# Performance work log

Measured on AMD Instinct MI355X. Metric: run time of the kernel, lower is better.

Reference implementation:

```python
import jax, jax.numpy as jnp
import numpy as np

N_USER = 805   # herbs
N_ITEM = 390   # symptoms
N = 1195       # total nodes
D = 64         # embedding_dim (forced by final matmul)
E = 1_000_000
E_SUB = 500_000
B = 2048
BN_EPS = 1e-5


def _gcn(x, W, b, edge):
    # GCNConv_SH: message = Linear(x_j), aggr='mean', then tanh.
    # Linear commutes with mean (bias included when in-degree>0; isolated nodes -> 0),
    # so transform nodes once, then gather->segment-mean.
    h = x @ W.T + b                      # [N, D]
    src, dst = edge[0], edge[1]
    agg = jax.ops.segment_sum(h[src], dst, num_segments=N)          # [N, D]
    cnt = jax.ops.segment_sum(jnp.ones(edge.shape[1], x.dtype), dst, num_segments=N)
    mean = agg / jnp.maximum(cnt, 1.0)[:, None]   # isolated nodes stay 0 (PyG mean aggr)
    return jnp.tanh(mean)


def _two_layer(x, W1, b1, W2, b2, edge):
    return _gcn(_gcn(x, W1, b1, edge), W2, b2, edge)


def _norm(x, axis):
    # self.Norm(emb, count, n_dim): L2 normalize along n_dim (0 for user side, 1 for item side)
    return x / jnp.linalg.norm(x, axis=axis, keepdims=True)


def setup_inputs() -> dict:
    key = jax.random.key(0)
    ks = jax.random.split(key, 12)
    emb = jax.random.normal(ks[0], (N, D), jnp.float32)
    s = 1.0 / np.sqrt(D)
    W1 = jax.random.normal(ks[1], (D, D), jnp.float32) * s
    b1 = jnp.zeros((D,), jnp.float32)
    W2 = jax.random.normal(ks[2], (D, D), jnp.float32) * s
    b2 = jnp.zeros((D,), jnp.float32)
    mlp_W = jax.random.normal(ks[3], (64, D), jnp.float32) * s
    mlp_b = jnp.zeros((64,), jnp.float32)
    bn_gamma = jnp.ones((64,), jnp.float32)
    bn_beta = jnp.zeros((64,), jnp.float32)
    # multi-hot prescription; guarantee nonzero row sums for the mean-pool divide
    presc = (jax.random.uniform(ks[4], (B, N_ITEM)) < 0.05).astype(jnp.float32)
    presc = presc.at[:, 0].set(1.0)
    total_g = jax.random.randint(ks[5], (2, E), 0, N)
    sub_g1 = jax.random.randint(ks[6], (2, E_SUB), 0, N)
    sub_g2 = jax.random.randint(ks[7], (2, E_SUB), 0, N)
    edge_index_SH = jax.random.randint(ks[8], (2, 1000), 0, N)
    return {"edge_index_SH": edge_index_SH, "prescription": presc,
            "emb": emb, "W1": W1, "b1": b1, "W2": W2, "b2": b2,
            "mlp_W": mlp_W, "mlp_b": mlp_b, "bn_gamma": bn_gamma, "bn_beta": bn_beta,
            "total_g": total_g, "sub_g1": sub_g1, "sub_g2": sub_g2}


def reference(edge_index_SH, prescription, emb, W1, b1, W2, b2, mlp_W, mlp_b,
              bn_gamma, bn_beta, total_g, sub_g1, sub_g2):
    # edge_index_SH is accepted (forward signature) but unused, as in the source.
    x_SH1 = emb                                   # SH_embedding(arange(1195))
    x_SH6 = _two_layer(emb, W1, b1, W2, b2, total_g)   # two shared GCNConv_SH layers
    SH_g3 = _two_layer(emb, W1, b1, W2, b2, sub_g1)
    SH_g33 = _two_layer(emb, W1, b1, W2, b2, sub_g2)

    # ssl_layer_loss returns normalized previous (raw-embedding) views
    s_u = _norm(x_SH1[:N_USER], 0)   # [805, D]
    s_i = _norm(x_SH1[N_USER:], 1)   # [390, D]
    # sgl_loss returns normalized sub-graph-1 views
    n_u = _norm(SH_g3[:N_USER], 0)
    n_i = _norm(SH_g3[N_USER:], 1)
    # Same2Loss (reconstructed): fuse all contrastive views into final node reps
    c_u = 0.25 * (s_i + n_i + _norm(x_SH6[N_USER:], 1) + _norm(SH_g33[N_USER:], 1))  # [390, D]
    c_i = 0.25 * (s_u + n_u + _norm(x_SH6[:N_USER], 0) + _norm(SH_g33[:N_USER], 0))  # [805, D]

    e_synd = prescription @ c_u                           # [B, D]
    e_synd = e_synd / prescription.sum(axis=1, keepdims=True)
    h = e_synd @ mlp_W.T + mlp_b                          # [B, 64]
    mu = h.mean(axis=0)
    var = h.var(axis=0)                                   # biased, as torch BN training
    h = (h - mu) / jnp.sqrt(var + BN_EPS) * bn_gamma + bn_beta
    h = jax.nn.relu(h)
    pre = h @ c_i.T                                       # [B, 805]
    return pre
```

## Files before the change

### kernel.cpp

```cpp
#include <hip/hip_runtime.h>
#include <hip/hip_bf16.h>


#define NN    1195
#define NUSER 805
#define NITEM 390
#define DD    64
#define BB    2048
#define NPAD  1216
#define E_TOT 1000000
#define E_SUB 500000
#define MT    19
#define KT    8
#define CHUNK 3
#define LSTR  72
#define OUT2STRIDE (NN*DD)
#define CPG    299
#define P8W    152
#define ROWS   96
#define RB     13
#define FNT    13
#define KPAD   448
#define ENT    7

typedef unsigned int uint;
typedef unsigned short u16;
typedef unsigned char u8;
typedef __attribute__((ext_vector_type(8))) short short8;
typedef __attribute__((ext_vector_type(4))) float f32x4;

__device__ __forceinline__ float wsum(float v) {
#pragma unroll
    for (int m = 32; m > 0; m >>= 1) v += __shfl_xor(v, m, 64);
    return v;
}
__device__ __forceinline__ u16 f2b(float f) {
    uint u = __float_as_uint(f);
    return (u16)((u + 0x7FFFu + ((u >> 16) & 1u)) >> 16);
}
__device__ __forceinline__ float b2f16(u16 b) { return __uint_as_float(((uint)b) << 16); }

#define CVT_EMB   0
#define CVT_W1    76480
#define CVT_B1    80576
#define CVT_W2    80640
#define CVT_B2    84736
#define CVT_MLPW  84800
#define CVT_MLPB  88896
#define CVT_GAMMA 88960
#define CVT_BETA  89024
#define CVT_TOTAL 89088

constexpr size_t alignUp64(size_t x) { return (x + 63) & ~size_t(63); }
constexpr size_t OFF_BNS  = 0;
constexpr size_t OFF_CNSS = 128;
constexpr size_t MEMSET_FLOATS = 384;
constexpr size_t OFF_FLAG = 384;
constexpr size_t OFF_CVT  = 448;
constexpr size_t OFF_ABF  = alignUp64(OFF_CVT + CVT_TOTAL);
constexpr size_t OFF_RC   = alignUp64(OFF_ABF + (3ull * NN * NPAD) / 2);
constexpr size_t OFF_POOL = alignUp64(OFF_RC + 3ull * NPAD);
constexpr size_t OFF_PART = OFF_POOL;
constexpr size_t OFF_H1   = alignUp64(OFF_PART + (size_t)KT * 3 * NPAD * 64);
constexpr size_t OFF_H2   = alignUp64(OFF_H1 + 64ull * NPAD);
constexpr size_t OFF_OUT2 = alignUp64(OFF_H2 + 3ull * 64 * NPAD);
constexpr size_t OFF_CU   = alignUp64(OFF_OUT2 + 3ull * NN * DD);
constexpr size_t OFF_CI   = alignUp64(OFF_CU + 448ull * DD);
constexpr size_t OFF_H    = alignUp64(OFF_CI + (size_t)NUSER * DD);
constexpr size_t POOL_END = alignUp64(OFF_H + (size_t)BB * DD);


__global__ __launch_bounds__(256) void k_cvt_all(const void* presc,
        const void* p1, const void* p2, const void* p3, const void* p4,
        const void* p5, const void* p6, const void* p7, const void* p8, const void* p9,
        float* __restrict__ dst, float* __restrict__ cnss, int* __restrict__ flag) {
    int isbf = (((const u16*)presc)[0] == 0x3F80u) ? 1 : 0;
    int t = threadIdx.x;
    int i = blockIdx.x * 256 + t;
    if (i == 0) *flag = isbf;
    const void* s2; int o2;
    if      (i < CVT_W1)    { s2 = p1; o2 = i; }
    else if (i < CVT_B1)    { s2 = p2; o2 = i - CVT_W1; }
    else if (i < CVT_W2)    { s2 = p3; o2 = i - CVT_B1; }
    else if (i < CVT_B2)    { s2 = p4; o2 = i - CVT_W2; }
    else if (i < CVT_MLPW)  { s2 = p5; o2 = i - CVT_B2; }
    else if (i < CVT_MLPB)  { s2 = p6; o2 = i - CVT_MLPW; }
    else if (i < CVT_GAMMA) { s2 = p7; o2 = i - CVT_MLPB; }
    else if (i < CVT_BETA)  { s2 = p8; o2 = i - CVT_GAMMA; }
    else                    { s2 = p9; o2 = i - CVT_BETA; }
    float v = isbf ? __bfloat162float(((const __hip_bfloat16*)s2)[o2])
                   : ((const float*)s2)[o2];
    dst[i] = v;
    float x2 = (i < NUSER * 64) ? v * v : 0.0f;
    __shared__ float sd[256];
    sd[t] = x2;
    __syncthreads();
    if (t < 64 && blockIdx.x * 256 < NUSER * 64) {
        float s = sd[t] + sd[t + 64] + sd[t + 128] + sd[t + 192];
        if (s != 0.0f) atomicAdd(&cnss[t], s);
    }
}

__global__ __launch_bounds__(512) void k_histp(const int* __restrict__ tg,
        const int* __restrict__ s1, const int* __restrict__ s2,
        uint* __restrict__ P8, int S) {
    __shared__ __align__(16) uint lds[ROWS * P8W];
    int b = blockIdx.x;
    int p = b % S;
    int rg = b / S;
    int r = rg % RB;
    int g = rg / RB;
    int r0 = r * ROWS;
    int t = threadIdx.x;

    {
        uint4* l4 = (uint4*)lds;
        for (int i = t; i < (ROWS * P8W) >> 2; i += 512) l4[i] = (uint4){0u, 0u, 0u, 0u};
    }
    __syncthreads();

    const int* eg = (g == 0) ? tg : (g == 1 ? s1 : s2);
    int Eg = (g == 0) ? E_TOT : E_SUB;
    int e0 = (int)(((long)p * Eg / S) & ~3L);
    int e1 = (p == S - 1) ? Eg : (int)(((long)(p + 1) * Eg / S) & ~3L);
    const int* srcp = eg;
    const int* dstp = eg + Eg;
    for (int i = e0 + t * 4; i < e1; i += 512 * 4) {
        int4 d4 = *(const int4*)(dstp + i);
        int4 s4 = *(const int4*)(srcp + i);
        int rw;
        rw = d4.x - r0; if ((unsigned)rw < ROWS) atomicAdd(&lds[rw * P8W + (s4.x >> 3)], 1u << ((s4.x & 7) * 4));
        rw = d4.y - r0; if ((unsigned)rw < ROWS) atomicAdd(&lds[rw * P8W + (s4.y >> 3)], 1u << ((s4.y & 7) * 4));
        rw = d4.z - r0; if ((unsigned)rw < ROWS) atomicAdd(&lds[rw * P8W + (s4.z >> 3)], 1u << ((s4.z & 7) * 4));
        rw = d4.w - r0; if ((unsigned)rw < ROWS) atomicAdd(&lds[rw * P8W + (s4.w >> 3)], 1u << ((s4.w & 7) * 4));
    }
    __syncthreads();

    int rmax = ROWS; if (r0 + rmax > NN) rmax = NN - r0;
    uint* out = P8 + ((size_t)p * 3 + g) * NN * P8W + (size_t)r0 * P8W;
    int n4 = (rmax * P8W) >> 2;
    const uint4* l4 = (const uint4*)lds;
    uint4* o4 = (uint4*)out;
    for (int i = t; i < n4; i += 512) o4[i] = l4[i];
}

__global__ __launch_bounds__(256) void k_abfrc(const uint* __restrict__ P8, int S,
        u16* __restrict__ Abf, float* __restrict__ rcnt) {
    int row = blockIdx.x;
    int g = row / NN, m = row % NN;
    int t = threadIdx.x, w = t >> 6;
    float partial = 0.0f;
    if (t < P8W) {
        uint cnt[8] = {0, 0, 0, 0, 0, 0, 0, 0};
        for (int p = 0; p < S; ++p) {
            uint v = P8[(((size_t)p * 3 + g) * NN + m) * P8W + t];
#pragma unroll
            for (int k = 0; k < 8; ++k) cnt[k] += (v >> (4 * k)) & 15u;
        }
        uint4 o;
        o.x = (uint)f2b((float)cnt[0]) | ((uint)f2b((float)cnt[1]) << 16);
        o.y = (uint)f2b((float)cnt[2]) | ((uint)f2b((float)cnt[3]) << 16);
        o.z = (uint)f2b((float)cnt[4]) | ((uint)f2b((float)cnt[5]) << 16);
        o.w = (uint)f2b((float)cnt[6]) | ((uint)f2b((float)cnt[7]) << 16);
        *(uint4*)(Abf + (size_t)row * NPAD + t * 8) = o;
#pragma unroll
        for (int k = 0; k < 8; ++k) partial += (float)cnt[k];
    }
    partial = wsum(partial);
    __shared__ float ws4[4];
    if ((t & 63) == 0) ws4[w] = partial;
    __syncthreads();
    if (t == 0)
        rcnt[g * NPAD + m] = 1.0f / fmaxf(ws4[0] + ws4[1] + ws4[2] + ws4[3], 1.0f);
}

__global__ __launch_bounds__(256) void k_xf2(const float* __restrict__ xsrc,
        size_t xgstride, int ngb, int rowlim,
        const float* __restrict__ W, const float* __restrict__ bias,
        u16* __restrict__ Hhi, u16* __restrict__ Hlo, size_t hgstride, int ostride) {
    int b = blockIdx.x;
    int g = b / ngb, nt = b % ngb;
    int n0 = nt * 64;
    int t = threadIdx.x, w = t >> 6, l = t & 63;
    __shared__ u16 Ah[64 * LSTR], Al[64 * LSTR], Bh[64 * LSTR], Bl[64 * LSTR];
    __shared__ float bs[64];
    if (t < 64) bs[t] = bias ? bias[t] : 0.0f;
    int r = t >> 2, c0 = (t & 3) * 16;
    {
        const float* Wr = W + r * 64 + c0;
        int node = n0 + r;
        const float* Xr = xsrc + xgstride * g + (size_t)node * 64 + c0;
        bool xv = node < rowlim;
#pragma unroll
        for (int j = 0; j < 4; ++j) {
            float4 wv = *(const float4*)(Wr + j * 4);
            float4 xw = xv ? *(const float4*)(Xr + j * 4) : (float4){0.f, 0.f, 0.f, 0.f};
            float a4[4] = {wv.x, wv.y, wv.z, wv.w};
            float b4[4] = {xw.x, xw.y, xw.z, xw.w};
            u16 ah[4], al[4], bh[4], bl[4];
#pragma unroll
            for (int jj = 0; jj < 4; ++jj) {
                ah[jj] = f2b(a4[jj]); al[jj] = f2b(a4[jj] - b2f16(ah[jj]));
                bh[jj] = f2b(b4[jj]); bl[jj] = f2b(b4[jj] - b2f16(bh[jj]));
            }
            uint2 pa, pb, pc, pd;
            pa.x = (uint)ah[0] | ((uint)ah[1] << 16); pa.y = (uint)ah[2] | ((uint)ah[3] << 16);
            pb.x = (uint)al[0] | ((uint)al[1] << 16); pb.y = (uint)al[2] | ((uint)al[3] << 16);
            pc.x = (uint)bh[0] | ((uint)bh[1] << 16); pc.y = (uint)bh[2] | ((uint)bh[3] << 16);
            pd.x = (uint)bl[0] | ((uint)bl[1] << 16); pd.y = (uint)bl[2] | ((uint)bl[3] << 16);
            int off = r * LSTR + c0 + j * 4;
            *(uint2*)(Ah + off) = pa;
            *(uint2*)(Al + off) = pb;
            *(uint2*)(Bh + off) = pc;
            *(uint2*)(Bl + off) = pd;
        }
    }
    __syncthreads();
    f32x4 acc[4];
#pragma unroll
    for (int p = 0; p < 4; ++p) acc[p] = (f32x4){0.f, 0.f, 0.f, 0.f};
    int mrow = w * 16 + (l & 15);
    int q8 = (l >> 4) * 8;
#pragma unroll
    for (int ks = 0; ks < 2; ++ks) {
        short8 ah = *(const short8*)(Ah + mrow * LSTR + ks * 32 + q8);
        short8 al = *(const short8*)(Al + mrow * LSTR + ks * 32 + q8);
#pragma unroll
        for (int p = 0; p < 4; ++p) {
            int nrow = p * 16 + (l & 15);
            short8 bh = *(const short8*)(Bh + nrow * LSTR + ks * 32 + q8);
            short8 bl = *(const short8*)(Bl + nrow * LSTR + ks * 32 + q8);
            acc[p] = __builtin_amdgcn_mfma_f32_16x16x32_bf16(ah, bh, acc[p], 0, 0, 0);
            acc[p] = __builtin_amdgcn_mfma_f32_16x16x32_bf16(ah, bl, acc[p], 0, 0, 0);
            acc[p] = __builtin_amdgcn_mfma_f32_16x16x32_bf16(al, bh, acc[p], 0, 0, 0);
        }
    }
    int q = l >> 4;
#pragma unroll
    for (int p = 0; p < 4; ++p) {
        int node = n0 + p * 16 + (l & 15);
#pragma unroll
        for (int rr2 = 0; rr2 < 4; ++rr2) {
            int d = w * 16 + q * 4 + rr2;
            float v = acc[p][rr2] + bs[d];
            u16 h = f2b(v);
            size_t o = hgstride * g + (size_t)d * ostride + node;
            Hhi[o] = h;
            Hlo[o] = f2b(v - b2f16(h));
        }
    }
}

__global__ __launch_bounds__(256) void k_aggp(const u16* __restrict__ Abf,
        const u16* __restrict__ Hhi, const u16* __restrict__ Hlo, size_t hstride,
        float* __restrict__ part) {
    int b = blockIdx.x;
    int kt = b & 7;
    int mt = (b >> 3) % MT;
    int g  = (b >> 3) / MT;
    int t = threadIdx.x, w = t >> 6, l = t & 63;
    __shared__ u16 As[64 * LSTR], Bh[64 * LSTR], Bl[64 * LSTR];
    f32x4 acc[4];
#pragma unroll
    for (int p = 0; p < 4; ++p) acc[p] = (f32x4){0.f, 0.f, 0.f, 0.f};
    int m0 = mt * 64;
    const u16* Ag = Abf + (size_t)g * NN * NPAD;
    const u16* Hg = Hhi + hstride * g;
    const u16* Lg = Hlo + hstride * g;
    int st0 = kt * CHUNK;
    int st1 = st0 + CHUNK; if (st1 > MT) st1 = MT;
    int rr = t >> 4, c4 = (t & 15) * 4;
    for (int st = st0; st < st1; ++st) {
        int s0 = st * 64;
        __syncthreads();
#pragma unroll
        for (int pass = 0; pass < 4; ++pass) {
            int r = pass * 16 + rr;
            uint2 av = {0u, 0u};
            if (m0 + r < NN) av = *(const uint2*)(Ag + (size_t)(m0 + r) * NPAD + s0 + c4);
            *(uint2*)(As + r * LSTR + c4) = av;
            *(uint2*)(Bh + r * LSTR + c4) = *(const uint2*)(Hg + (size_t)r * NPAD + s0 + c4);
            *(uint2*)(Bl + r * LSTR + c4) = *(const uint2*)(Lg + (size_t)r * NPAD + s0 + c4);
        }
        __syncthreads();
        int mrow = w * 16 + (l & 15);
        int q8 = (l >> 4) * 8;
#pragma unroll
        for (int ks = 0; ks < 2; ++ks) {
            short8 a = *(const short8*)(As + mrow * LSTR + ks * 32 + q8);
#pragma unroll
            for (int p = 0; p < 4; ++p) {
                int nrow = p * 16 + (l & 15);
                short8 bh = *(const short8*)(Bh + nrow * LSTR + ks * 32 + q8);
                short8 bl = *(const short8*)(Bl + nrow * LSTR + ks * 32 + q8);
                acc[p] = __builtin_amdgcn_mfma_f32_16x16x32_bf16(a, bh, acc[p], 0, 0, 0);
                acc[p] = __builtin_amdgcn_mfma_f32_16x16x32_bf16(a, bl, acc[p], 0, 0, 0);
            }
        }
    }
    int q = l >> 4;
#pragma unroll
    for (int p = 0; p < 4; ++p) {
        int n = p * 16 + (l & 15);
#pragma unroll
        for (int r = 0; r < 4; ++r) {
            int m = m0 + w * 16 + q * 4 + r;
            if (m < NN)
                part[(((size_t)kt * 3 + g) * NPAD + m) * 64 + n] = acc[p][r];
        }
    }
}

__global__ __launch_bounds__(256) void k_comb1(const float* __restrict__ part,
        const float* __restrict__ rcnt, float* __restrict__ h1) {
    int g = blockIdx.x / CPG, bi = blockIdx.x % CPG;
    int idx = bi * 256 + threadIdx.x;
    if (idx >= NN * 64) return;
    int m = idx >> 6;
    float s = 0.0f;
#pragma unroll
    for (int k = 0; k < KT; ++k)
        s += part[(((size_t)k * 3 + g) * NPAD + m) * 64 + (idx & 63)];
    h1[(size_t)g * NN * 64 + idx] = tanhf(s * rcnt[g * NPAD + m]);
}

__global__ __launch_bounds__(256) void k_comb(const float* __restrict__ part,
        const float* __restrict__ rcnt, float* __restrict__ out, float* __restrict__ cnss) {
    int g = blockIdx.x / CPG, bi = blockIdx.x % CPG;
    int t = threadIdx.x;
    int idx = bi * 256 + t;
    int m = idx >> 6, n = idx & 63;
    bool valid = idx < NN * 64;
    float v = 0.0f;
    if (valid) {
        float s = 0.0f;
#pragma unroll
        for (int k = 0; k < KT; ++k)
            s += part[(((size_t)k * 3 + g) * NPAD + m) * 64 + n];
        v = tanhf(s * rcnt[g * NPAD + m]);
        out[(size_t)g * NN * 64 + idx] = v;
    }
    float x2 = (valid && m < NUSER) ? v * v : 0.0f;
    __shared__ float sd[256];
    sd[t] = x2;
    __syncthreads();
    if (t < 64) {
        float s = sd[t] + sd[t + 64] + sd[t + 128] + sd[t + 192];
        if (s != 0.0f) atomicAdd(&cnss[(g + 1) * 64 + t], s);
    }
}

__global__ void k_cuci(const float* __restrict__ embf, const float* __restrict__ out2,
                       const float* __restrict__ cnss, float* __restrict__ cu,
                       float* __restrict__ ci) {
    int b = blockIdx.x, l = threadIdx.x;
    if (b < 448) {
        if (b >= NITEM) { cu[(size_t)b * DD + l] = 0.0f; return; }
        int node = NUSER + b;
        const float* v0 = embf + (size_t)node * DD;
        const float* v1 = out2 + (size_t)node * DD;
        const float* v2 = out2 + OUT2STRIDE + (size_t)node * DD;
        const float* v3 = out2 + 2ull * OUT2STRIDE + (size_t)node * DD;
        float total = 0.0f;
        { float x = v0[l]; float ss = wsum(x * x); total += x / sqrtf(ss); }
        { float x = v1[l]; float ss = wsum(x * x); total += x / sqrtf(ss); }
        { float x = v2[l]; float ss = wsum(x * x); total += x / sqrtf(ss); }
        { float x = v3[l]; float ss = wsum(x * x); total += x / sqrtf(ss); }
        cu[(size_t)b * DD + l] = 0.25f * total;
    } else {
        int u = b - 448;
        size_t i = (size_t)u * DD + l;
        float s = embf[i] / sqrtf(cnss[l])
                + out2[i] / sqrtf(cnss[64 + l])
                + out2[OUT2STRIDE + i] / sqrtf(cnss[128 + l])
                + out2[2ull * OUT2STRIDE + i] / sqrtf(cnss[192 + l]);
        ci[i] = 0.25f * s;
    }
}

__global__ __launch_bounds__(256) void k_esynd(const void* __restrict__ presc,
        const u16* __restrict__ cwh, const u16* __restrict__ cwl,
        const float* __restrict__ mlpB, const int* __restrict__ flag,
        float* __restrict__ hpre, float* __restrict__ bnsum) {
    int m0 = blockIdx.x * 64;
    int t = threadIdx.x, w = t >> 6, l = t & 63;
    int isbf = *flag;
    const u16* pB = (const u16*)presc;
    const float* pF = (const float*)presc;
    __shared__ u16 As[64 * LSTR], Bh[64 * LSTR], Bl[64 * LSTR];
    __shared__ u16 Ones[16 * LSTR];
    __shared__ float bs[64];
    __shared__ float r1[4][64], r2[4][64];
    for (int i = t; i < 16 * LSTR; i += 256) Ones[i] = (i < 64) ? 0x3F80u : 0u;
    if (t < 64) bs[t] = mlpB[t];

    f32x4 acc[4], acc1;
#pragma unroll
    for (int p = 0; p < 4; ++p) acc[p] = (f32x4){0.f, 0.f, 0.f, 0.f};
    acc1 = (f32x4){0.f, 0.f, 0.f, 0.f};

    int rr = t >> 4, c4 = (t & 15) * 4;
    for (int st = 0; st < ENT; ++st) {
        int s0 = st * 64;
        __syncthreads();
#pragma unroll
        for (int pass = 0; pass < 4; ++pass) {
            int r = pass * 16 + rr;
            int m = m0 + r;
            int kb = s0 + c4;
            u16 a4[4];
            if (kb + 3 < NITEM) {
                if (isbf) {
                    const uint* p32 = (const uint*)pB + (((size_t)m * NITEM + kb) >> 1);
                    uint u0 = p32[0], u1 = p32[1];
                    a4[0] = (u16)u0; a4[1] = (u16)(u0 >> 16);
                    a4[2] = (u16)u1; a4[3] = (u16)(u1 >> 16);
                } else {
                    const float2* pf2 = (const float2*)(pF + (size_t)m * NITEM + kb);
                    float2 f0 = pf2[0], f1 = pf2[1];
                    a4[0] = f2b(f0.x); a4[1] = f2b(f0.y);
                    a4[2] = f2b(f1.x); a4[3] = f2b(f1.y);
                }
            } else {
#pragma unroll
                for (int j = 0; j < 4; ++j) {
                    int k = kb + j;
                    a4[j] = (k < NITEM)
                          ? (isbf ? pB[(size_t)m * NITEM + k] : f2b(pF[(size_t)m * NITEM + k]))
                          : (u16)0;
                }
            }
            uint2 o;
            o.x = (uint)a4[0] | ((uint)a4[1] << 16);
            o.y = (uint)a4[2] | ((uint)a4[3] << 16);
            *(uint2*)(As + r * LSTR + c4) = o;
            *(uint2*)(Bh + r * LSTR + c4) = *(const uint2*)(cwh + (size_t)r * KPAD + s0 + c4);
            *(uint2*)(Bl + r * LSTR + c4) = *(const uint2*)(cwl + (size_t)r * KPAD + s0 + c4);
        }
        __syncthreads();
        int mrow = w * 16 + (l & 15);
        int q8 = (l >> 4) * 8;
#pragma unroll
        for (int ks = 0; ks < 2; ++ks) {
            short8 a = *(const short8*)(As + mrow * LSTR + ks * 32 + q8);
            short8 on = *(const short8*)(Ones + (l & 15) * LSTR + ks * 32 + q8);
            acc1 = __builtin_amdgcn_mfma_f32_16x16x32_bf16(a, on, acc1, 0, 0, 0);
#pragma unroll
            for (int p = 0; p < 4; ++p) {
                int nrow = p * 16 + (l & 15);
                short8 bh = *(const short8*)(Bh + nrow * LSTR + ks * 32 + q8);
                short8 bl = *(const short8*)(Bl + nrow * LSTR + ks * 32 + q8);
                acc[p] = __builtin_amdgcn_mfma_f32_16x16x32_bf16(a, bh, acc[p], 0, 0, 0);
                acc[p] = __builtin_amdgcn_mfma_f32_16x16x32_bf16(a, bl, acc[p], 0, 0, 0);
            }
        }
    }
    float inv[4];
#pragma unroll
    for (int r = 0; r < 4; ++r)
        inv[r] = 1.0f / __shfl(acc1[r], l & 48, 64);
    int q = l >> 4;
#pragma unroll
    for (int p = 0; p < 4; ++p) {
        int col = p * 16 + (l & 15);
        float a = 0.0f, c = 0.0f;
#pragma unroll
        for (int r = 0; r < 4; ++r) {
            float hv = acc[p][r] * inv[r] + bs[col];
            hpre[(size_t)(m0 + w * 16 + q * 4 + r) * DD + col] = hv;
            a += hv; c = fmaf(hv, hv, c);
        }
        a += __shfl_xor(a, 16, 64); a += __shfl_xor(a, 32, 64);
        c += __shfl_xor(c, 16, 64); c += __shfl_xor(c, 32, 64);
        if (l < 16) { r1[w][col] = a; r2[w][col] = c; }
    }
    __syncthreads();
    if (t < 64) {
        atomicAdd(&bnsum[t],      r1[0][t] + r1[1][t] + r1[2][t] + r1[3][t]);
        atomicAdd(&bnsum[64 + t], r2[0][t] + r2[1][t] + r2[2][t] + r2[3][t]);
    }
}

__global__ __launch_bounds__(256) void k_final(const float* __restrict__ hpre,
        const float* __restrict__ bnsum, const float* __restrict__ gamma,
        const float* __restrict__ beta, const float* __restrict__ ci,
        void* __restrict__ out, const int* __restrict__ flag) {
    int b = blockIdx.x;
    int mt = b / FNT, nt = b % FNT;
    int m0 = mt * 64, n0 = nt * 64;
    int t = threadIdx.x, w = t >> 6, l = t & 63;
    __shared__ u16 Ah[64 * LSTR], Al[64 * LSTR], Bh[64 * LSTR], Bl[64 * LSTR];
    __shared__ float mn[64], rsg[64], bt[64];
    if (t < 64) {
        float mean = bnsum[t] * (1.0f / BB);
        float var = bnsum[64 + t] * (1.0f / BB) - mean * mean;
        mn[t] = mean;
        rsg[t] = gamma[t] / sqrtf(var + 1e-5f);
        bt[t] = beta[t];
    }
    __syncthreads();
    const float4* hp4 = (const float4*)(hpre + (size_t)m0 * 64);
    const float4* ci4 = (const float4*)ci;
#pragma unroll
    for (int k = 0; k < 4; ++k) {
        int i = t + k * 256;
        int r = i >> 4, c4 = (i & 15) * 4;
        float4 v = hp4[i];
        float vv[4] = {v.x, v.y, v.z, v.w};
        u16 hh[4], ll[4];
#pragma unroll
        for (int j = 0; j < 4; ++j) {
            int d = c4 + j;
            float x = fmaxf((vv[j] - mn[d]) * rsg[d] + bt[d], 0.0f);
            u16 hb = f2b(x);
            hh[j] = hb;
            ll[j] = f2b(x - b2f16(hb));
        }
        uint2 ph, pl;
        ph.x = (uint)hh[0] | ((uint)hh[1] << 16);
        ph.y = (uint)hh[2] | ((uint)hh[3] << 16);
        pl.x = (uint)ll[0] | ((uint)ll[1] << 16);
        pl.y = (uint)ll[2] | ((uint)ll[3] << 16);
        *(uint2*)(Ah + r * LSTR + c4) = ph;
        *(uint2*)(Al + r * LSTR + c4) = pl;
        int col = n0 + r;
        float4 cv = (col < NUSER) ? ci4[(size_t)col * 16 + (i & 15)]
                                  : (float4){0.f, 0.f, 0.f, 0.f};
        float cc[4] = {cv.x, cv.y, cv.z, cv.w};
#pragma unroll
        for (int j = 0; j < 4; ++j) {
            u16 hb = f2b(cc[j]);
            hh[j] = hb;
            ll[j] = f2b(cc[j] - b2f16(hb));
        }
        ph.x = (uint)hh[0] | ((uint)hh[1] << 16);
        ph.y = (uint)hh[2] | ((uint)hh[3] << 16);
        pl.x = (uint)ll[0] | ((uint)ll[1] << 16);
        pl.y = (uint)ll[2] | ((uint)ll[3] << 16);
        *(uint2*)(Bh + r * LSTR + c4) = ph;
        *(uint2*)(Bl + r * LSTR + c4) = pl;
    }
    __syncthreads();
    f32x4 acc[4];
#pragma unroll
    for (int p = 0; p < 4; ++p) acc[p] = (f32x4){0.f, 0.f, 0.f, 0.f};
    int mrow = w * 16 + (l & 15);
    int q8 = (l >> 4) * 8;
#pragma unroll
    for (int ks = 0; ks < 2; ++ks) {
        short8 ah = *(const short8*)(Ah + mrow * LSTR + ks * 32 + q8);
        short8 al = *(const short8*)(Al + mrow * LSTR + ks * 32 + q8);
#pragma unroll
        for (int p = 0; p < 4; ++p) {
            int nrow = p * 16 + (l & 15);
            short8 bh = *(const short8*)(Bh + nrow * LSTR + ks * 32 + q8);
            short8 bl = *(const short8*)(Bl + nrow * LSTR + ks * 32 + q8);
            acc[p] = __builtin_amdgcn_mfma_f32_16x16x32_bf16(ah, bh, acc[p], 0, 0, 0);
            acc[p] = __builtin_amdgcn_mfma_f32_16x16x32_bf16(ah, bl, acc[p], 0, 0, 0);
            acc[p] = __builtin_amdgcn_mfma_f32_16x16x32_bf16(al, bh, acc[p], 0, 0, 0);
        }
    }
    int isbf = *flag;
    int q = l >> 4;
#pragma unroll
    for (int p = 0; p < 4; ++p) {
        int col = n0 + p * 16 + (l & 15);
        if (col < NUSER) {
#pragma unroll
            for (int r = 0; r < 4; ++r) {
                int row = m0 + w * 16 + q * 4 + r;
                size_t o = (size_t)row * NUSER + col;
                if (isbf) ((__hip_bfloat16*)out)[o] = __float2bfloat16(acc[p][r]);
                else      ((float*)out)[o] = acc[p][r];
            }
        }
    }
}

extern "C" void kernel_launch(void* const* d_in, const int* in_sizes, int n_in,
                              void* d_out, int out_size, void* d_ws, size_t ws_size,
                              hipStream_t stream) {
    const void* presc = d_in[1];
    const void* emb   = d_in[2];
    const void* W1    = d_in[3];
    const void* b1    = d_in[4];
    const void* W2    = d_in[5];
    const void* b2    = d_in[6];
    const void* mlpW  = d_in[7];
    const void* mlpB  = d_in[8];
    const void* gamma = d_in[9];
    const void* beta  = d_in[10];
    const int* tg = (const int*)d_in[11];
    const int* s1 = (const int*)d_in[12];
    const int* s2 = (const int*)d_in[13];
    float* ws = (float*)d_ws;
    (void)in_sizes; (void)n_in; (void)out_size;

    float* bnsum = ws + OFF_BNS;
    float* cnss  = ws + OFF_CNSS;
    int*   flag  = (int*)(ws + OFF_FLAG);
    float* cvt   = ws + OFF_CVT;
    float* embF  = cvt + CVT_EMB;
    float* W1F   = cvt + CVT_W1;
    float* b1F   = cvt + CVT_B1;
    float* W2F   = cvt + CVT_W2;
    float* b2F   = cvt + CVT_B2;
    float* mlpWF = cvt + CVT_MLPW;
    float* mlpBF = cvt + CVT_MLPB;
    float* gamF  = cvt + CVT_GAMMA;
    float* betF  = cvt + CVT_BETA;
    u16*   Abf   = (u16*)(ws + OFF_ABF);
    float* rcnt  = ws + OFF_RC;
    uint*  P8    = (uint*)(ws + OFF_POOL);
    float* part  = ws + OFF_PART;
    u16*   H1hi  = (u16*)(ws + OFF_H1);
    u16*   H1lo  = H1hi + 64ull * NPAD;
    u16*   H2hi  = (u16*)(ws + OFF_H2);
    u16*   H2lo  = H2hi + 3ull * 64 * NPAD;
    float* out2  = ws + OFF_OUT2;
    float* cu    = ws + OFF_CU;
    float* ci    = ws + OFF_CI;
    float* hpre  = ws + OFF_H;
    u16*   cwh   = (u16*)(ws + OFF_PART);
    u16*   cwl   = cwh + 64ull * KPAD;

    size_t p8per = 3ull * NN * P8W;
    int S = 4;
    if      (ws_size >= (OFF_POOL + 16ull * p8per) * 4) S = 16;
    else if (ws_size >= (OFF_POOL +  8ull * p8per) * 4) S = 8;

    hipMemsetAsync(ws, 0, MEMSET_FLOATS * sizeof(float), stream);
    k_cvt_all<<<CVT_TOTAL / 256, 256, 0, stream>>>(
        presc, emb, W1, b1, W2, b2, mlpW, mlpB, gamma, beta, cvt, cnss, flag);

    k_histp<<<3 * RB * S, 512, 0, stream>>>(tg, s1, s2, P8, S);
    k_abfrc<<<3 * NN, 256, 0, stream>>>(P8, S, Abf, rcnt);

    k_xf2<<<MT, 256, 0, stream>>>(embF, 0, MT, NN, W1F, b1F, H1hi, H1lo, 0, NPAD);
    k_aggp<<<3 * MT * KT, 256, 0, stream>>>(Abf, H1hi, H1lo, 0, part);
    k_comb1<<<3 * CPG, 256, 0, stream>>>(part, rcnt, out2);
    k_xf2<<<3 * MT, 256, 0, stream>>>(out2, (size_t)NN * 64, MT, NN, W2F, b2F,
                                      H2hi, H2lo, 64ull * NPAD, NPAD);
    k_aggp<<<3 * MT * KT, 256, 0, stream>>>(Abf, H2hi, H2lo, 64ull * NPAD, part);
    k_comb<<<3 * CPG, 256, 0, stream>>>(part, rcnt, out2, cnss);

    k_cuci<<<448 + NUSER, 64, 0, stream>>>(embF, out2, cnss, cu, ci);
    k_xf2<<<ENT, 256, 0, stream>>>(cu, 0, ENT, 448, mlpWF, nullptr, cwh, cwl, 0, KPAD);

    k_esynd<<<BB / 64, 256, 0, stream>>>(presc, cwh, cwl, mlpBF, flag, hpre, bnsum);
    k_final<<<(BB / 64) * FNT, 256, 0, stream>>>(hpre, bnsum, gamF, betF, ci, d_out, flag);
}
```

Baseline: 215.9 us.

## Fuse front-end kernels and fold layer-1 combine into second transform

Merges the memset, conversion, histogram and embedding-norm work into one heterogeneous front kernel. It also fuses adjacency-to-bf16 conversion with the first linear transform, and folds the layer-1 partial reduction plus tanh into the layer-2 transform's input load. The intent is to remove several kernel launches and an intermediate write and read of the layer-1 output. The trade-offs are a serial single-block column-norm reduction and a larger, more divergent kernel.

```diff
diff --git a/kernel.cpp b/kernel.cpp
--- a/kernel.cpp
+++ b/kernel.cpp
@@ -39,6 +39,20 @@
     return (u16)((u + 0x7FFFu + ((u >> 16) & 1u)) >> 16);
 }
 __device__ __forceinline__ float b2f16(u16 b) { return __uint_as_float(((uint)b) << 16); }
+__device__ __forceinline__ void split4(const float* v, u16* hh, u16* ll) {
+#pragma unroll
+    for (int j = 0; j < 4; ++j) {
+        u16 h = f2b(v[j]);
+        hh[j] = h;
+        ll[j] = f2b(v[j] - b2f16(h));
+    }
+}
+__device__ __forceinline__ uint2 pack4(const u16* x) {
+    uint2 o;
+    o.x = (uint)x[0] | ((uint)x[1] << 16);
+    o.y = (uint)x[2] | ((uint)x[3] << 16);
+    return o;
+}
 
 #define CVT_EMB   0
 #define CVT_W1    76480
@@ -54,7 +68,6 @@
 constexpr size_t alignUp64(size_t x) { return (x + 63) & ~size_t(63); }
 constexpr size_t OFF_BNS  = 0;
 constexpr size_t OFF_CNSS = 128;
-constexpr size_t MEMSET_FLOATS = 384;
 constexpr size_t OFF_FLAG = 384;
 constexpr size_t OFF_CVT  = 448;
 constexpr size_t OFF_ABF  = alignUp64(OFF_CVT + CVT_TOTAL);
@@ -70,149 +83,149 @@
 constexpr size_t POOL_END = alignUp64(OFF_H + (size_t)BB * DD);
 
 
-__global__ __launch_bounds__(256) void k_cvt_all(const void* presc,
+__global__ __launch_bounds__(512) void k_front(const void* presc, const void* emb,
         const void* p1, const void* p2, const void* p3, const void* p4,
         const void* p5, const void* p6, const void* p7, const void* p8, const void* p9,
-        float* __restrict__ dst, float* __restrict__ cnss, int* __restrict__ flag) {
+        const int* __restrict__ tg, const int* __restrict__ s1, const int* __restrict__ s2,
+        float* __restrict__ dst, float* __restrict__ cnss, float* __restrict__ bnsum,
+        int* __restrict__ flag, uint* __restrict__ P8, int S, int HB) {
+    __shared__ __align__(16) uint lds[ROWS * P8W];
+    int b = blockIdx.x, t = threadIdx.x;
     int isbf = (((const u16*)presc)[0] == 0x3F80u) ? 1 : 0;
-    int t = threadIdx.x;
-    int i = blockIdx.x * 256 + t;
-    if (i == 0) *flag = isbf;
-    const void* s2; int o2;
-    if      (i < CVT_W1)    { s2 = p1; o2 = i; }
-    else if (i < CVT_B1)    { s2 = p2; o2 = i - CVT_W1; }
-    else if (i < CVT_W2)    { s2 = p3; o2 = i - CVT_B1; }
-    else if (i < CVT_B2)    { s2 = p4; o2 = i - CVT_W2; }
-    else if (i < CVT_MLPW)  { s2 = p5; o2 = i - CVT_B2; }
-    else if (i < CVT_MLPB)  { s2 = p6; o2 = i - CVT_MLPW; }
-    else if (i < CVT_GAMMA) { s2 = p7; o2 = i - CVT_MLPB; }
-    else if (i < CVT_BETA)  { s2 = p8; o2 = i - CVT_GAMMA; }
-    else                    { s2 = p9; o2 = i - CVT_BETA; }
-    float v = isbf ? __bfloat162float(((const __hip_bfloat16*)s2)[o2])
-                   : ((const float*)s2)[o2];
-    dst[i] = v;
-    float x2 = (i < NUSER * 64) ? v * v : 0.0f;
-    __shared__ float sd[256];
-    sd[t] = x2;
-    __syncthreads();
-    if (t < 64 && blockIdx.x * 256 < NUSER * 64) {
-        float s = sd[t] + sd[t + 64] + sd[t + 128] + sd[t + 192];
-        if (s != 0.0f) atomicAdd(&cnss[t], s);
-    }
-}
-
-__global__ __launch_bounds__(512) void k_histp(const int* __restrict__ tg,
-        const int* __restrict__ s1, const int* __restrict__ s2,
-        uint* __restrict__ P8, int S) {
-    __shared__ __align__(16) uint lds[ROWS * P8W];
-    int b = blockIdx.x;
-    int p = b % S;
-    int rg = b / S;
-    int r = rg % RB;
-    int g = rg / RB;
-    int r0 = r * ROWS;
-    int t = threadIdx.x;
-
-    {
-        uint4* l4 = (uint4*)lds;
-        for (int i = t; i < (ROWS * P8W) >> 2; i += 512) l4[i] = (uint4){0u, 0u, 0u, 0u};
-    }
-    __syncthreads();
-
-    const int* eg = (g == 0) ? tg : (g == 1 ? s1 : s2);
-    int Eg = (g == 0) ? E_TOT : E_SUB;
-    int e0 = (int)(((long)p * Eg / S) & ~3L);
-    int e1 = (p == S - 1) ? Eg : (int)(((long)(p + 1) * Eg / S) & ~3L);
-    const int* srcp = eg;
-    const int* dstp = eg + Eg;
-    for (int i = e0 + t * 4; i < e1; i += 512 * 4) {
-        int4 d4 = *(const int4*)(dstp + i);
-        int4 s4 = *(const int4*)(srcp + i);
-        int rw;
-        rw = d4.x - r0; if ((unsigned)rw < ROWS) atomicAdd(&lds[rw * P8W + (s4.x >> 3)], 1u << ((s4.x & 7) * 4));
-        rw = d4.y - r0; if ((unsigned)rw < ROWS) atomicAdd(&lds[rw * P8W + (s4.y >> 3)], 1u << ((s4.y & 7) * 4));
-        rw = d4.z - r0; if ((unsigned)rw < ROWS) atomicAdd(&lds[rw * P8W + (s4.z >> 3)], 1u << ((s4.z & 7) * 4));
-        rw = d4.w - r0; if ((unsigned)rw < ROWS) atomicAdd(&lds[rw * P8W + (s4.w >> 3)], 1u << ((s4.w & 7) * 4));
-    }
-    __syncthreads();
-
-    int rmax = ROWS; if (r0 + rmax > NN) rmax = NN - r0;
-    uint* out = P8 + ((size_t)p * 3 + g) * NN * P8W + (size_t)r0 * P8W;
-    int n4 = (rmax * P8W) >> 2;
-    const uint4* l4 = (const uint4*)lds;
-    uint4* o4 = (uint4*)out;
-    for (int i = t; i < n4; i += 512) o4[i] = l4[i];
-}
-
-__global__ __launch_bounds__(256) void k_abfrc(const uint* __restrict__ P8, int S,
-        u16* __restrict__ Abf, float* __restrict__ rcnt) {
-    int row = blockIdx.x;
-    int g = row / NN, m = row % NN;
-    int t = threadIdx.x, w = t >> 6;
-    float partial = 0.0f;
-    if (t < P8W) {
-        uint cnt[8] = {0, 0, 0, 0, 0, 0, 0, 0};
-        for (int p = 0; p < S; ++p) {
-            uint v = P8[(((size_t)p * 3 + g) * NN + m) * P8W + t];
-#pragma unroll
-            for (int k = 0; k < 8; ++k) cnt[k] += (v >> (4 * k)) & 15u;
-        }
-        uint4 o;
-        o.x = (uint)f2b((float)cnt[0]) | ((uint)f2b((float)cnt[1]) << 16);
-        o.y = (uint)f2b((float)cnt[2]) | ((uint)f2b((float)cnt[3]) << 16);
-        o.z = (uint)f2b((float)cnt[4]) | ((uint)f2b((float)cnt[5]) << 16);
-        o.w = (uint)f2b((float)cnt[6]) | ((uint)f2b((float)cnt[7]) << 16);
-        *(uint4*)(Abf + (size_t)row * NPAD + t * 8) = o;
-#pragma unroll
-        for (int k = 0; k < 8; ++k) partial += (float)cnt[k];
-    }
-    partial = wsum(partial);
-    __shared__ float ws4[4];
-    if ((t & 63) == 0) ws4[w] = partial;
-    __syncthreads();
-    if (t == 0)
-        rcnt[g * NPAD + m] = 1.0f / fmaxf(ws4[0] + ws4[1] + ws4[2] + ws4[3], 1.0f);
-}
-
-__global__ __launch_bounds__(256) void k_xf2(const float* __restrict__ xsrc,
-        size_t xgstride, int ngb, int rowlim,
-        const float* __restrict__ W, const float* __restrict__ bias,
-        u16* __restrict__ Hhi, u16* __restrict__ Hlo, size_t hgstride, int ostride) {
-    int b = blockIdx.x;
-    int g = b / ngb, nt = b % ngb;
-    int n0 = nt * 64;
-    int t = threadIdx.x, w = t >> 6, l = t & 63;
-    __shared__ u16 Ah[64 * LSTR], Al[64 * LSTR], Bh[64 * LSTR], Bl[64 * LSTR];
-    __shared__ float bs[64];
+    if (b < HB) {
+        int p = b % S;
+        int rg = b / S;
+        int r = rg % RB;
+        int g = rg / RB;
+        int r0 = r * ROWS;
+        {
+            uint4* l4 = (uint4*)lds;
+            for (int i = t; i < (ROWS * P8W) >> 2; i += 512) l4[i] = (uint4){0u, 0u, 0u, 0u};
+        }
+        __syncthreads();
+        const int* eg = (g == 0) ? tg : (g == 1 ? s1 : s2);
+        int Eg = (g == 0) ? E_TOT : E_SUB;
+        int e0 = (int)(((long)p * Eg / S) & ~3L);
+        int e1 = (p == S - 1) ? Eg : (int)(((long)(p + 1) * Eg / S) & ~3L);
+        const int* srcp = eg;
+        const int* dstp = eg + Eg;
+        for (int i = e0 + t * 4; i < e1; i += 512 * 4) {
+            int4 d4 = *(const int4*)(dstp + i);
+            int4 s4 = *(const int4*)(srcp + i);
+            int rw;
+            rw = d4.x - r0; if ((unsigned)rw < ROWS) atomicAdd(&lds[rw * P8W + (s4.x >> 3)], 1u << ((s4.x & 7) * 4));
+            rw = d4.y - r0; if ((unsigned)rw < ROWS) atomicAdd(&lds[rw * P8W + (s4.y >> 3)], 1u << ((s4.y & 7) * 4));
+            rw = d4.z - r0; if ((unsigned)rw < ROWS) atomicAdd(&lds[rw * P8W + (s4.z >> 3)], 1u << ((s4.z & 7) * 4));
+            rw = d4.w - r0; if ((unsigned)rw < ROWS) atomicAdd(&lds[rw * P8W + (s4.w >> 3)], 1u << ((s4.w & 7) * 4));
+        }
+        __syncthreads();
+        int rmax = ROWS; if (r0 + rmax > NN) rmax = NN - r0;
+        uint* out = P8 + ((size_t)p * 3 + g) * NN * P8W + (size_t)r0 * P8W;
+        int n4 = (rmax * P8W) >> 2;
+        const uint4* l4 = (const uint4*)lds;
+        uint4* o4 = (uint4*)out;
+        for (int i = t; i < n4; i += 512) o4[i] = l4[i];
+    } else if (b == HB) {
+        for (int i = t; i < 192; i += 512) cnss[64 + i] = 0.0f;
+        if (t < 128) bnsum[t] = 0.0f;
+        int c = t & 63, chunk = t >> 6;
+        float s = 0.0f;
+        const u16* e16 = (const u16*)emb;
+        const float* e32 = (const float*)emb;
+        for (int r = chunk; r < NUSER; r += 8) {
+            float v = isbf ? b2f16(e16[r * 64 + c]) : e32[r * 64 + c];
+            s = fmaf(v, v, s);
+        }
+        float* sd = (float*)lds;
+        sd[t] = s;
+        __syncthreads();
+        if (t < 64) {
+            float tot = 0.0f;
+#pragma unroll
+            for (int j = 0; j < 8; ++j) tot += sd[j * 64 + t];
+            cnss[t] = tot;
+        }
+    } else {
+        int i = (b - HB - 1) * 512 + t;
+        if (i == 0) *flag = isbf;
+        if (i < CVT_TOTAL) {
+            const void* s2p; int o2;
+            if      (i < CVT_W1)    { s2p = p1; o2 = i; }
+            else if (i < CVT_B1)    { s2p = p2; o2 = i - CVT_W1; }
+            else if (i < CVT_W2)    { s2p = p3; o2 = i - CVT_B1; }
+            else if (i < CVT_B2)    { s2p = p4; o2 = i - CVT_W2; }
+            else if (i < CVT_MLPW)  { s2p = p5; o2 = i - CVT_B2; }
+            else if (i < CVT_MLPB)  { s2p = p6; o2 = i - CVT_MLPW; }
+            else if (i < CVT_GAMMA) { s2p = p7; o2 = i - CVT_MLPB; }
+            else if (i < CVT_BETA)  { s2p = p8; o2 = i - CVT_GAMMA; }
+            else                    { s2p = p9; o2 = i - CVT_BETA; }
+            dst[i] = isbf ? __bfloat162float(((const __hip_bfloat16*)s2p)[o2])
+                          : ((const float*)s2p)[o2];
+        }
+    }
+}
+
+__device__ __forceinline__ void xf2_body(int g, int n0, int t,
+        const float* xsrc, size_t xgstride,
+        const float* part, const float* rcnt, int fromPart, int rowlim,
+        const float* W, const float* bias,
+        u16* Hhi, u16* Hlo, size_t hgstride, int ostride,
+        u16* Ah, u16* Al, u16* Bh, u16* Bl, float* bs) {
+    int w = t >> 6, l = t & 63;
     if (t < 64) bs[t] = bias ? bias[t] : 0.0f;
     int r = t >> 2, c0 = (t & 3) * 16;
     {
         const float* Wr = W + r * 64 + c0;
+        float av[16];
+#pragma unroll
+        for (int j4 = 0; j4 < 4; ++j4) {
+            float4 v = *(const float4*)(Wr + j4 * 4);
+            av[j4*4+0] = v.x; av[j4*4+1] = v.y; av[j4*4+2] = v.z; av[j4*4+3] = v.w;
+        }
+#pragma unroll
+        for (int j4 = 0; j4 < 4; ++j4) {
+            u16 hh[4], ll[4];
+            split4(av + j4*4, hh, ll);
+            *(uint2*)(Ah + r * LSTR + c0 + j4*4) = pack4(hh);
+            *(uint2*)(Al + r * LSTR + c0 + j4*4) = pack4(ll);
+        }
+    }
+    {
         int node = n0 + r;
-        const float* Xr = xsrc + xgstride * g + (size_t)node * 64 + c0;
-        bool xv = node < rowlim;
-#pragma unroll
-        for (int j = 0; j < 4; ++j) {
-            float4 wv = *(const float4*)(Wr + j * 4);
-            float4 xw = xv ? *(const float4*)(Xr + j * 4) : (float4){0.f, 0.f, 0.f, 0.f};
-            float a4[4] = {wv.x, wv.y, wv.z, wv.w};
-            float b4[4] = {xw.x, xw.y, xw.z, xw.w};
-            u16 ah[4], al[4], bh[4], bl[4];
-#pragma unroll
-            for (int jj = 0; jj < 4; ++jj) {
-                ah[jj] = f2b(a4[jj]); al[jj] = f2b(a4[jj] - b2f16(ah[jj]));
-                bh[jj] = f2b(b4[jj]); bl[jj] = f2b(b4[jj] - b2f16(bh[jj]));
+        float xr[16];
+#pragma unroll
+        for (int j = 0; j < 16; ++j) xr[j] = 0.0f;
+        if (node < rowlim) {
+            if (fromPart) {
+#pragma unroll
+                for (int k = 0; k < KT; ++k) {
+                    const float* pp = part + (((size_t)k * 3 + g) * NPAD + node) * 64 + c0;
+#pragma unroll
+                    for (int j4 = 0; j4 < 4; ++j4) {
+                        float4 v = *(const float4*)(pp + j4 * 4);
+                        xr[j4*4+0] += v.x; xr[j4*4+1] += v.y;
+                        xr[j4*4+2] += v.z; xr[j4*4+3] += v.w;
+                    }
+                }
+                float rc = rcnt[g * NPAD + node];
+#pragma unroll
+                for (int j = 0; j < 16; ++j) xr[j] = tanhf(xr[j] * rc);
+            } else {
+                const float* Xr = xsrc + xgstride * g + (size_t)node * 64 + c0;
+#pragma unroll
+                for (int j4 = 0; j4 < 4; ++j4) {
+                    float4 v = *(const float4*)(Xr + j4 * 4);
+                    xr[j4*4+0] = v.x; xr[j4*4+1] = v.y;
+                    xr[j4*4+2] = v.z; xr[j4*4+3] = v.w;
+                }
             }
-            uint2 pa, pb, pc, pd;
-            pa.x = (uint)ah[0] | ((uint)ah[1] << 16); pa.y = (uint)ah[2] | ((uint)ah[3] << 16);
-            pb.x = (uint)al[0] | ((uint)al[1] << 16); pb.y = (uint)al[2] | ((uint)al[3] << 16);
-            pc.x = (uint)bh[0] | ((uint)bh[1] << 16); pc.y = (uint)bh[2] | ((uint)bh[3] << 16);
-            pd.x = (uint)bl[0] | ((uint)bl[1] << 16); pd.y = (uint)bl[2] | ((uint)bl[3] << 16);
-            int off = r * LSTR + c0 + j * 4;
-            *(uint2*)(Ah + off) = pa;
-            *(uint2*)(Al + off) = pb;
-            *(uint2*)(Bh + off) = pc;
-            *(uint2*)(Bl + off) = pd;
+        }
+#pragma unroll
+        for (int j4 = 0; j4 < 4; ++j4) {
+            u16 hh[4], ll[4];
+            split4(xr + j4*4, hh, ll);
+            *(uint2*)(Bh + r * LSTR + c0 + j4*4) = pack4(hh);
+            *(uint2*)(Bl + r * LSTR + c0 + j4*4) = pack4(ll);
         }
     }
     __syncthreads();
@@ -248,6 +261,59 @@
             Hhi[o] = h;
             Hlo[o] = f2b(v - b2f16(h));
         }
+    }
+}
+
+__global__ __launch_bounds__(256) void k_xf2(const float* __restrict__ xsrc,
+        size_t xgstride, const float* __restrict__ part, const float* __restrict__ rcnt,
+        int fromPart, int ngb, int rowlim,
+        const float* __restrict__ W, const float* __restrict__ bias,
+        u16* __restrict__ Hhi, u16* __restrict__ Hlo, size_t hgstride, int ostride) {
+    __shared__ u16 Ah[64 * LSTR], Al[64 * LSTR], Bh[64 * LSTR], Bl[64 * LSTR];
+    __shared__ float bs[64];
+    int b = blockIdx.x;
+    xf2_body(b / ngb, (b % ngb) * 64, threadIdx.x, xsrc, xgstride, part, rcnt,
+             fromPart, rowlim, W, bias, Hhi, Hlo, hgstride, ostride,
+             Ah, Al, Bh, Bl, bs);
+}
+
+__global__ __launch_bounds__(256) void k_abf_xf1(const uint* __restrict__ P8, int S,
+        u16* __restrict__ Abf, float* __restrict__ rcnt,
+        const float* __restrict__ embF, const float* __restrict__ W1,
+        const float* __restrict__ b1, u16* __restrict__ H1hi, u16* __restrict__ H1lo) {
+    __shared__ u16 Ah[64 * LSTR], Al[64 * LSTR], Bh[64 * LSTR], Bl[64 * LSTR];
+    __shared__ float bs[64];
+    __shared__ float ws4[4];
+    int b = blockIdx.x, t = threadIdx.x;
+    if (b < 3 * NN) {
+        int g = b / NN, m = b % NN;
+        int w = t >> 6;
+        float partial = 0.0f;
+        if (t < P8W) {
+            uint cnt[8] = {0, 0, 0, 0, 0, 0, 0, 0};
+            for (int p = 0; p < S; ++p) {
+                uint v = P8[(((size_t)p * 3 + g) * NN + m) * P8W + t];
+#pragma unroll
+                for (int k = 0; k < 8; ++k) cnt[k] += (v >> (4 * k)) & 15u;
+            }
+            uint4 o;
+            o.x = (uint)f2b((float)cnt[0]) | ((uint)f2b((float)cnt[1]) << 16);
+            o.y = (uint)f2b((float)cnt[2]) | ((uint)f2b((float)cnt[3]) << 16);
+            o.z = (uint)f2b((float)cnt[4]) | ((uint)f2b((float)cnt[5]) << 16);
+            o.w = (uint)f2b((float)cnt[6]) | ((uint)f2b((float)cnt[7]) << 16);
+            *(uint4*)(Abf + (size_t)b * NPAD + t * 8) = o;
+#pragma unroll
+            for (int k = 0; k < 8; ++k) partial += (float)cnt[k];
+        }
+        partial = wsum(partial);
+        if ((t & 63) == 0) ws4[w] = partial;
+        __syncthreads();
+        if (t == 0)
+            rcnt[g * NPAD + m] = 1.0f / fmaxf(ws4[0] + ws4[1] + ws4[2] + ws4[3], 1.0f);
+    } else {
+        int nt = b - 3 * NN;
+        xf2_body(0, nt * 64, t, embF, 0, nullptr, nullptr, 0, NN, W1, b1,
+                 H1hi, H1lo, 0, NPAD, Ah, Al, Bh, Bl, bs);
     }
 }
 
@@ -309,19 +375,6 @@
                 part[(((size_t)kt * 3 + g) * NPAD + m) * 64 + n] = acc[p][r];
         }
     }
-}
-
-__global__ __launch_bounds__(256) void k_comb1(const float* __restrict__ part,
-        const float* __restrict__ rcnt, float* __restrict__ h1) {
-    int g = blockIdx.x / CPG, bi = blockIdx.x % CPG;
-    int idx = bi * 256 + threadIdx.x;
-    if (idx >= NN * 64) return;
-    int m = idx >> 6;
-    float s = 0.0f;
-#pragma unroll
-    for (int k = 0; k < KT; ++k)
-        s += part[(((size_t)k * 3 + g) * NPAD + m) * 64 + (idx & 63)];
-    h1[(size_t)g * NN * 64 + idx] = tanhf(s * rcnt[g * NPAD + m]);
 }
 
 __global__ __launch_bounds__(256) void k_comb(const float* __restrict__ part,
@@ -516,29 +569,15 @@
             hh[j] = hb;
             ll[j] = f2b(x - b2f16(hb));
         }
-        uint2 ph, pl;
-        ph.x = (uint)hh[0] | ((uint)hh[1] << 16);
-        ph.y = (uint)hh[2] | ((uint)hh[3] << 16);
-        pl.x = (uint)ll[0] | ((uint)ll[1] << 16);
-        pl.y = (uint)ll[2] | ((uint)ll[3] << 16);
-        *(uint2*)(Ah + r * LSTR + c4) = ph;
-        *(uint2*)(Al + r * LSTR + c4) = pl;
+        *(uint2*)(Ah + r * LSTR + c4) = pack4(hh);
+        *(uint2*)(Al + r * LSTR + c4) = pack4(ll);
         int col = n0 + r;
         float4 cv = (col < NUSER) ? ci4[(size_t)col * 16 + (i & 15)]
                                   : (float4){0.f, 0.f, 0.f, 0.f};
         float cc[4] = {cv.x, cv.y, cv.z, cv.w};
-#pragma unroll
-        for (int j = 0; j < 4; ++j) {
-            u16 hb = f2b(cc[j]);
-            hh[j] = hb;
-            ll[j] = f2b(cc[j] - b2f16(hb));
-        }
-        ph.x = (uint)hh[0] | ((uint)hh[1] << 16);
-        ph.y = (uint)hh[2] | ((uint)hh[3] << 16);
-        pl.x = (uint)ll[0] | ((uint)ll[1] << 16);
-        pl.y = (uint)ll[2] | ((uint)ll[3] << 16);
-        *(uint2*)(Bh + r * LSTR + c4) = ph;
-        *(uint2*)(Bl + r * LSTR + c4) = pl;
+        split4(cc, hh, ll);
+        *(uint2*)(Bh + r * LSTR + c4) = pack4(hh);
+        *(uint2*)(Bl + r * LSTR + c4) = pack4(ll);
     }
     __syncthreads();
     f32x4 acc[4];
@@ -628,25 +667,22 @@
     int S = 4;
     if      (ws_size >= (OFF_POOL + 16ull * p8per) * 4) S = 16;
     else if (ws_size >= (OFF_POOL +  8ull * p8per) * 4) S = 8;
-
-    hipMemsetAsync(ws, 0, MEMSET_FLOATS * sizeof(float), stream);
-    k_cvt_all<<<CVT_TOTAL / 256, 256, 0, stream>>>(
-        presc, emb, W1, b1, W2, b2, mlpW, mlpB, gamma, beta, cvt, cnss, flag);
-
-    k_histp<<<3 * RB * S, 512, 0, stream>>>(tg, s1, s2, P8, S);
-    k_abfrc<<<3 * NN, 256, 0, stream>>>(P8, S, Abf, rcnt);
-
-    k_xf2<<<MT, 256, 0, stream>>>(embF, 0, MT, NN, W1F, b1F, H1hi, H1lo, 0, NPAD);
+    int HB = 3 * RB * S;
+    int CVTB = CVT_TOTAL / 512;
+
+    k_front<<<HB + 1 + CVTB, 512, 0, stream>>>(presc, emb,
+        emb, W1, b1, W2, b2, mlpW, mlpB, gamma, beta,
+        tg, s1, s2, cvt, cnss, bnsum, flag, P8, S, HB);
+    k_abf_xf1<<<3 * NN + MT, 256, 0, stream>>>(P8, S, Abf, rcnt,
+        embF, W1F, b1F, H1hi, H1lo);
     k_aggp<<<3 * MT * KT, 256, 0, stream>>>(Abf, H1hi, H1lo, 0, part);
-    k_comb1<<<3 * CPG, 256, 0, stream>>>(part, rcnt, out2);
-    k_xf2<<<3 * MT, 256, 0, stream>>>(out2, (size_t)NN * 64, MT, NN, W2F, b2F,
-                                      H2hi, H2lo, 64ull * NPAD, NPAD);
+    k_xf2<<<3 * MT, 256, 0, stream>>>(nullptr, 0, part, rcnt, 1, MT, NN,
+        W2F, b2F, H2hi, H2lo, 64ull * NPAD, NPAD);
     k_aggp<<<3 * MT * KT, 256, 0, stream>>>(Abf, H2hi, H2lo, 64ull * NPAD, part);
     k_comb<<<3 * CPG, 256, 0, stream>>>(part, rcnt, out2, cnss);
-
     k_cuci<<<448 + NUSER, 64, 0, stream>>>(embF, out2, cnss, cu, ci);
-    k_xf2<<<ENT, 256, 0, stream>>>(cu, 0, ENT, 448, mlpWF, nullptr, cwh, cwl, 0, KPAD);
-
+    k_xf2<<<ENT, 256, 0, stream>>>(cu, 0, nullptr, nullptr, 0, ENT, 448,
+        mlpWF, nullptr, cwh, cwl, 0, KPAD);
     k_esynd<<<BB / 64, 256, 0, stream>>>(presc, cwh, cwl, mlpBF, flag, hpre, bnsum);
     k_final<<<(BB / 64) * FNT, 256, 0, stream>>>(hpre, bnsum, gamF, betF, ci, d_out, flag);
 }
```

Measured after the change: 229.6 us. +6.4%, slower.
